# Performance work log

Hardware: AMD Instinct MI355X
Metric: run time of the kernel (lower is better)

## Reference

```python
import jax, jax.numpy as jnp
import numpy as np

N = 50000
E = 800000
F_IN = 128
HID = 16
HEADS = 8
CLS = 16
NEG_SLOPE = 0.2


def setup_inputs() -> dict:
    key = jax.random.key(0)
    ks = jax.random.split(key, 12)
    x = jax.random.normal(ks[0], (N, F_IN), dtype=jnp.float32)
    edge_index = jax.random.randint(ks[1], (2, E), 0, N, dtype=jnp.int32)
    s = 0.1
    W1 = jax.random.normal(ks[2], (F_IN, HEADS * HID), dtype=jnp.float32) * s
    att_src1 = jax.random.normal(ks[3], (HEADS, HID), dtype=jnp.float32) * s
    att_dst1 = jax.random.normal(ks[4], (HEADS, HID), dtype=jnp.float32) * s
    b1 = jax.random.normal(ks[5], (HEADS * HID,), dtype=jnp.float32) * s
    W2 = jax.random.normal(ks[6], (HEADS * HID, CLS), dtype=jnp.float32) * s
    att_src2 = jax.random.normal(ks[7], (1, CLS), dtype=jnp.float32) * s
    att_dst2 = jax.random.normal(ks[8], (1, CLS), dtype=jnp.float32) * s
    b2 = jax.random.normal(ks[9], (CLS,), dtype=jnp.float32) * s
    return {"x": x, "edge_index": edge_index, "W1": W1, "att_src1": att_src1,
            "att_dst1": att_dst1, "b1": b1, "W2": W2, "att_src2": att_src2,
            "att_dst2": att_dst2, "b2": b2}


def _gat_conv(x, src, dst, W, a_src, a_dst, b, heads, out_ch, concat):
    n = x.shape[0]
    h = (x @ W).reshape(n, heads, out_ch)                     # [N,H,C]
    alpha_src = (h * a_src[None]).sum(-1)                     # [N,H]
    alpha_dst = (h * a_dst[None]).sum(-1)                     # [N,H]
    e = jax.nn.leaky_relu(alpha_src[src] + alpha_dst[dst], NEG_SLOPE)  # [E,H]
    m = jax.lax.stop_gradient(jax.ops.segment_max(e, dst, num_segments=n))
    e = jnp.exp(e - m[dst])
    denom = jax.ops.segment_sum(e, dst, num_segments=n)
    alpha = e / (denom[dst] + 1e-16)                          # [E,H]
    msg = h[src] * alpha[:, :, None]                          # [E,H,C]
    out = jax.ops.segment_sum(msg, dst, num_segments=n)       # [N,H,C]
    out = out.reshape(n, heads * out_ch) if concat else out.mean(axis=1)
    return out + b


def reference(x, edge_index, W1, att_src1, att_dst1, b1, W2, att_src2, att_dst2, b2):
    # PyG GATConv default add_self_loops=True
    loop = jnp.arange(N, dtype=edge_index.dtype)
    src = jnp.concatenate([edge_index[0], loop])
    dst = jnp.concatenate([edge_index[1], loop])
    h = _gat_conv(x, src, dst, W1, att_src1, att_dst1, b1, HEADS, HID, True)
    h = jax.nn.elu(h)
    # dropout inactive (eval mode)
    out = _gat_conv(h, src, dst, W2, att_src2, att_dst2, b2, 1, CLS, False)
    return out
```

## Files before the change

### kernel.cpp

```cpp
#include <hip/hip_runtime.h>
#include <hip/hip_bf16.h>
#include <limits.h>
#include <math.h>

#define N 50000
#define E_ 800000
#define ETOT 850000
#define HH 128
#define HEADS 8
#define HID 16
#define CLS 16
#define NEG 0.2f
#define NB ((N + 255) / 256)

typedef unsigned short u16;
typedef unsigned int   u32;
typedef unsigned long long u64;
typedef short s8v __attribute__((ext_vector_type(8)));
typedef float f4v __attribute__((ext_vector_type(4)));

__device__ __forceinline__ u16 f2bu(float f){
  union{float f; u32 i;} c; c.f = f;
  u32 lsb = (c.i >> 16) & 1u;
  c.i += 0x7fffu + lsb;
  return (u16)(c.i >> 16);
}
__device__ __forceinline__ float bu2f(u16 u){
  union{u32 i; float f;} c; c.i = ((u32)u) << 16; return c.f;
}
__device__ __forceinline__ float blo(u32 u){ union{u32 i; float f;} c; c.i = u << 16; return c.f; }
__device__ __forceinline__ float bhi(u32 u){ union{u32 i; float f;} c; c.i = u & 0xffff0000u; return c.f; }

__global__ __launch_bounds__(256) void k_prepW(const float* __restrict__ W,
                                               u16* __restrict__ wth, u16* __restrict__ wtl){
  int i = blockIdx.x*256 + threadIdx.x;
  if(i >= 128*128) return;
  int k = i >> 7, c = i & 127;
  float v = W[i];
  u16 hi = f2bu(v);
  u16 lo = f2bu(v - bu2f(hi));
  wth[c*128 + k] = hi;
  wtl[c*128 + k] = lo;
}

__global__ __launch_bounds__(256) void k_link(const int* __restrict__ ei,
                                              int* __restrict__ head,
                                              int* __restrict__ srcv,
                                              int* __restrict__ nxt){
  int e = blockIdx.x*256 + threadIdx.x;
  if(e >= ETOT) return;
  int s, d;
  if(e < E_){ s = ei[e]; d = ei[E_ + e]; } else { s = d = e - E_; }
  int old = atomicExch(&head[d], e);
  srcv[e] = s;
  nxt[e]  = old;
}

#define GBM 64
__global__ __launch_bounds__(256) void k_gemm1m(const float* __restrict__ x,
                                                const u16* __restrict__ wth,
                                                const u16* __restrict__ wtl,
                                                u16* __restrict__ h1b){
  __shared__ u16 xh[GBM][40], xl[GBM][40];
  __shared__ u16 wh[128][40], wl[128][40];
  int tid  = threadIdx.x;
  int wv   = tid >> 6;
  int lane = tid & 63;
  int row0 = blockIdx.x * GBM;

  f4v acc[4][2];
  #pragma unroll
  for(int t=0;t<4;t++)
    #pragma unroll
    for(int u=0;u<2;u++) acc[t][u] = (f4v){0.f,0.f,0.f,0.f};

  int xr  = tid >> 2;
  int xkq = (tid & 3) * 8;
  int wc  = tid & 127;
  int wq  = (tid >> 7) * 8;
  int xrow = row0 + xr; if(xrow >= N) xrow = N-1;
  const float* xb = x + (size_t)xrow*128 + xkq;
  int fr = lane & 15, fg = lane >> 4;
  int kk = fg*8;

  for(int kc=0; kc<4; kc++){
    int k0 = kc*32;
    float4 v0 = *(const float4*)(xb + k0);
    float4 v1 = *(const float4*)(xb + k0 + 4);
    __syncthreads();
    {
      float vv[8] = {v0.x,v0.y,v0.z,v0.w,v1.x,v1.y,v1.z,v1.w};
      s8v H, L;
      #pragma unroll
      for(int j=0;j<8;j++){
        u16 h_ = f2bu(vv[j]);
        H[j] = (short)h_;
        L[j] = (short)f2bu(vv[j] - bu2f(h_));
      }
      *(s8v*)&xh[xr][xkq] = H;
      *(s8v*)&xl[xr][xkq] = L;
    }
    #pragma unroll
    for(int j=0;j<2;j++){
      int kq = wq + j*16;
      *(s8v*)&wh[wc][kq] = *(const s8v*)&wth[wc*128 + k0 + kq];
      *(s8v*)&wl[wc][kq] = *(const s8v*)&wtl[wc*128 + k0 + kq];
    }
    __syncthreads();
    s8v a_h[4], a_l[4], b_h[2], b_l[2];
    #pragma unroll
    for(int t=0;t<4;t++){
      a_h[t] = *(const s8v*)&xh[t*16 + fr][kk];
      a_l[t] = *(const s8v*)&xl[t*16 + fr][kk];
    }
    #pragma unroll
    for(int u=0;u<2;u++){
      int col = wv*32 + u*16 + fr;
      b_h[u] = *(const s8v*)&wh[col][kk];
      b_l[u] = *(const s8v*)&wl[col][kk];
    }
    #pragma unroll
    for(int t=0;t<4;t++){
      #pragma unroll
      for(int u=0;u<2;u++){
        acc[t][u] = __builtin_amdgcn_mfma_f32_16x16x32_bf16(a_h[t], b_h[u], acc[t][u], 0,0,0);
        acc[t][u] = __builtin_amdgcn_mfma_f32_16x16x32_bf16(a_h[t], b_l[u], acc[t][u], 0,0,0);
        acc[t][u] = __builtin_amdgcn_mfma_f32_16x16x32_bf16(a_l[t], b_h[u], acc[t][u], 0,0,0);
      }
    }
  }
  #pragma unroll
  for(int t=0;t<4;t++){
    #pragma unroll
    for(int j=0;j<4;j++){
      int row = row0 + t*16 + fg*4 + j;
      if(row < N){
        u16* dst = h1b + (size_t)row*128 + wv*32 + fr;
        dst[0]  = f2bu(acc[t][0][j]);
        dst[16] = f2bu(acc[t][1][j]);
      }
    }
  }
}

__global__ __launch_bounds__(256) void k_alpha1(const u16* __restrict__ h1b,
                                                const float* __restrict__ Asv,
                                                const float* __restrict__ Adv,
                                                float* __restrict__ as1,
                                                float* __restrict__ ad1){
  int id = blockIdx.x*256 + threadIdx.x;
  if(id >= N*HEADS) return;
  int i = id >> 3, h = id & 7;
  const uint4* hv = (const uint4*)(h1b + (size_t)i*HH + h*HID);
  uint4 u0 = hv[0], u1 = hv[1];
  float vals[16] = {blo(u0.x),bhi(u0.x),blo(u0.y),bhi(u0.y),
                    blo(u0.z),bhi(u0.z),blo(u0.w),bhi(u0.w),
                    blo(u1.x),bhi(u1.x),blo(u1.y),bhi(u1.y),
                    blo(u1.z),bhi(u1.z),blo(u1.w),bhi(u1.w)};
  float s=0.f, d=0.f;
  #pragma unroll
  for(int j=0;j<16;j++){
    s = fmaf(vals[j], Asv[h*HID+j], s);
    d = fmaf(vals[j], Adv[h*HID+j], d);
  }
  as1[id]=s; ad1[id]=d;
}

__global__ __launch_bounds__(256) void k_scan1walk(const int* __restrict__ head,
                                                   const int* __restrict__ nxt,
                                                   int* __restrict__ deg,
                                                   int* __restrict__ bsum){
  __shared__ int sm[256];
  int t = threadIdx.x;
  int i = blockIdx.x*256 + t;
  int cnt = 0;
  if(i < N){
    int e = head[i];
    while(e >= 0){ cnt++; e = nxt[e]; }
    deg[i] = cnt;
  }
  sm[t] = cnt;
  __syncthreads();
  #pragma unroll
  for(int ofs=128; ofs>0; ofs>>=1){
    if(t < ofs) sm[t] += sm[t+ofs];
    __syncthreads();
  }
  if(t == 0) bsum[blockIdx.x] = sm[0];
}

__global__ __launch_bounds__(256) void k_scan2(const int* __restrict__ bsum,
                                               int* __restrict__ boff,
                                               int* __restrict__ off){
  __shared__ int sm[256];
  int t = threadIdx.x;
  sm[t] = (t < NB) ? bsum[t] : 0;
  __syncthreads();
  #pragma unroll
  for(int ofs=1; ofs<256; ofs<<=1){
    int v = sm[t];
    int add = (t >= ofs) ? sm[t-ofs] : 0;
    __syncthreads();
    sm[t] = v + add;
    __syncthreads();
  }
  if(t < NB) boff[t] = (t == 0) ? 0 : sm[t-1];
  if(t == 255) off[N] = sm[NB-1];
}

__global__ __launch_bounds__(256) void k_scan3walk(const int* __restrict__ deg,
                                                   const int* __restrict__ boff,
                                                   const int* __restrict__ head,
                                                   const int* __restrict__ srcv,
                                                   const int* __restrict__ nxt,
                                                   int* __restrict__ off,
                                                   int* __restrict__ csr){
  __shared__ int sm[256];
  int t = threadIdx.x;
  int i = blockIdx.x*256 + t;
  int v0 = (i < N) ? deg[i] : 0;
  sm[t] = v0;
  __syncthreads();
  #pragma unroll
  for(int ofs=1; ofs<256; ofs<<=1){
    int v = sm[t];
    int add = (t >= ofs) ? sm[t-ofs] : 0;
    __syncthreads();
    sm[t] = v + add;
    __syncthreads();
  }
  if(i < N){
    int excl = boff[blockIdx.x] + sm[t] - v0;
    off[i] = excl;
    int e = head[i];
    int pos = excl;
    while(e >= 0){
      csr[pos++] = srcv[e];
      e = nxt[e];
    }
  }
}

#define CH 32
__global__ __launch_bounds__(256) void k_agg1(const int* __restrict__ off,
                                              const int* __restrict__ csr,
                                              const float* __restrict__ as1,
                                              const float* __restrict__ ad1,
                                              const u32* __restrict__ h1w,
                                              const float* __restrict__ b1,
                                              u32* __restrict__ helu_w){
  __shared__ float wsm[4][CH*8];
  __shared__ int   ssm[4][CH];
  int wv   = threadIdx.x >> 6;
  int lane = threadIdx.x & 63;
  int node = blockIdx.x*4 + wv;
  int beg = off[node], end = off[node+1];
  int h  = lane >> 3;
  int hh = lane & 7;
  int el = lane >> 3;
  float advA = ad1[node*8 + hh];
  float den = 0.f, num0 = 0.f, num1 = 0.f;
  float* wsw = wsm[wv];
  int*   ssw = ssm[wv];
  for(int base = beg; base < end; base += CH){
    int cnt = end - base; if(cnt > CH) cnt = CH;
    #pragma unroll
    for(int k=0;k<CH;k+=8){
      int e = el + k;
      if(e < cnt){
        int s = csr[base+e];
        if(hh == 0) ssw[e] = s;
        float v = as1[s*8+hh] + advA;
        v = v > 0.f ? v : NEG*v;
        wsw[e*8+hh] = __expf(v);
      }
    }
    int e = 0;
    for(; e+4 <= cnt; e += 4){
      int s0 = ssw[e], s1 = ssw[e+1], s2 = ssw[e+2], s3 = ssw[e+3];
      float w0 = wsw[e*8+h], w1 = wsw[e*8+8+h], w2 = wsw[e*8+16+h], w3 = wsw[e*8+24+h];
      u32 u0 = h1w[(size_t)s0*64 + lane];
      u32 u1 = h1w[(size_t)s1*64 + lane];
      u32 u2 = h1w[(size_t)s2*64 + lane];
      u32 u3 = h1w[(size_t)s3*64 + lane];
      den += (w0+w1)+(w2+w3);
      num0 = fmaf(w0, blo(u0), num0); num1 = fmaf(w0, bhi(u0), num1);
      num0 = fmaf(w1, blo(u1), num0); num1 = fmaf(w1, bhi(u1), num1);
      num0 = fmaf(w2, blo(u2), num0); num1 = fmaf(w2, bhi(u2), num1);
      num0 = fmaf(w3, blo(u3), num0); num1 = fmaf(w3, bhi(u3), num1);
    }
    for(; e < cnt; e++){
      int s = ssw[e];
      float w = wsw[e*8+h];
      u32 u = h1w[(size_t)s*64 + lane];
      den += w;
      num0 = fmaf(w, blo(u), num0);
      num1 = fmaf(w, bhi(u), num1);
    }
  }
  float2 bb = ((const float2*)b1)[lane];
  float inv = 1.f / (den + 1e-16f);
  float r0 = num0*inv + bb.x;
  float r1 = num1*inv + bb.y;
  r0 = r0 > 0.f ? r0 : expm1f(r0);
  r1 = r1 > 0.f ? r1 : expm1f(r1);
  helu_w[(size_t)node*64 + lane] = (u32)f2bu(r0) | ((u32)f2bu(r1) << 16);
}

__global__ __launch_bounds__(256) void k_gemm2(const u16* __restrict__ hb,
                                               const float* __restrict__ W2,
                                               const float* __restrict__ Asv,
                                               const float* __restrict__ Adv,
                                               u16* __restrict__ h2b,
                                               float* __restrict__ as2,
                                               float* __restrict__ ad2){
  __shared__ float Wl[128*16];
  int tid = threadIdx.x;
  const float4* W4 = (const float4*)W2;
  float4* Wl4 = (float4*)Wl;
  Wl4[tid]       = W4[tid];
  Wl4[tid + 256] = W4[tid + 256];
  __syncthreads();
  int i = blockIdx.x*16 + (tid >> 4);
  int c = tid & 15;
  if(i >= N) return;
  const uint4* h8 = (const uint4*)(hb + (size_t)i*HH);
  float acc = 0.f;
  #pragma unroll
  for(int ch=0; ch<16; ch++){
    uint4 u = h8[ch];
    int k = ch*8;
    acc = fmaf(blo(u.x), Wl[(k+0)*16+c], acc);
    acc = fmaf(bhi(u.x), Wl[(k+1)*16+c], acc);
    acc = fmaf(blo(u.y), Wl[(k+2)*16+c], acc);
    acc = fmaf(bhi(u.y), Wl[(k+3)*16+c], acc);
    acc = fmaf(blo(u.z), Wl[(k+4)*16+c], acc);
    acc = fmaf(bhi(u.z), Wl[(k+5)*16+c], acc);
    acc = fmaf(blo(u.w), Wl[(k+6)*16+c], acc);
    acc = fmaf(bhi(u.w), Wl[(k+7)*16+c], acc);
  }
  h2b[(size_t)i*CLS + c] = f2bu(acc);
  float ps = acc * Asv[c];
  float pd = acc * Adv[c];
  ps += __shfl_xor(ps,1); ps += __shfl_xor(ps,2); ps += __shfl_xor(ps,4); ps += __shfl_xor(ps,8);
  pd += __shfl_xor(pd,1); pd += __shfl_xor(pd,2); pd += __shfl_xor(pd,4); pd += __shfl_xor(pd,8);
  if(c == 0){ as2[i] = ps; ad2[i] = pd; }
}

__global__ __launch_bounds__(256) void k_agg2(const int* __restrict__ off,
                                              const int* __restrict__ csr,
                                              const float* __restrict__ as2,
                                              const float* __restrict__ ad2,
                                              const u32* __restrict__ h2w,
                                              const float* __restrict__ b2,
                                              float* __restrict__ outp){
  int t = threadIdx.x;
  int node = blockIdx.x*32 + (t >> 3);
  int c2 = t & 7;
  if(node >= N) return;
  int beg = off[node], end = off[node+1];
  float adv = ad2[node];
  float den = 0.f, num0 = 0.f, num1 = 0.f;
  for(int base = beg; base < end; base += 8){
    int cnt = end - base; if(cnt > 8) cnt = 8;
    float w_my = 0.f; int s_my = 0;
    if(c2 < cnt){
      s_my = csr[base + c2];
      float v = as2[s_my] + adv;
      v = v > 0.f ? v : NEG*v;
      w_my = __expf(v);
    }
    #pragma unroll
    for(int j=0; j<8; j++){
      if(j >= cnt) break;
      int src = (t & 56) | j;
      float w = __shfl(w_my, src);
      int   s = __shfl(s_my, src);
      u32 u = h2w[(size_t)s*8 + c2];
      den += w;
      num0 = fmaf(w, blo(u), num0);
      num1 = fmaf(w, bhi(u), num1);
    }
  }
  float inv = 1.f / (den + 1e-16f);
  float2 bb = ((const float2*)b2)[c2];
  float2 r;
  r.x = num0*inv + bb.x;
  r.y = num1*inv + bb.y;
  ((float2*)outp)[(size_t)node*8 + c2] = r;
}

extern "C" void kernel_launch(void* const* d_in, const int* in_sizes, int n_in,
                              void* d_out, int out_size, void* d_ws, size_t ws_size,
                              hipStream_t stream){
  const float* x     = (const float*)d_in[0];
  const int*   ei    = (const int*)  d_in[1];
  const float* W1    = (const float*)d_in[2];
  const float* av_s1 = (const float*)d_in[3];
  const float* av_d1 = (const float*)d_in[4];
  const float* b1    = (const float*)d_in[5];
  const float* W2    = (const float*)d_in[6];
  const float* av_s2 = (const float*)d_in[7];
  const float* av_d2 = (const float*)d_in[8];
  const float* b2    = (const float*)d_in[9];
  float* outp = (float*)d_out;

  char* p = (char*)d_ws;
  auto alloc = [&](size_t bytes){ char* q = p; p += (bytes + 255) & ~(size_t)255; return q; };
  u16*   h1b    = (u16*)  alloc((size_t)N*HH*2);
  u16*   helu_b = (u16*)  alloc((size_t)N*HH*2);
  u16*   h2b    = (u16*)  alloc((size_t)N*CLS*2);
  float* as1    = (float*)alloc((size_t)N*HEADS*4);
  float* ad1    = (float*)alloc((size_t)N*HEADS*4);
  float* as2    = (float*)alloc((size_t)N*4);
  float* ad2    = (float*)alloc((size_t)N*4);
  int*   deg    = (int*)  alloc((size_t)N*4);
  int*   head   = (int*)  alloc((size_t)N*4);
  int*   off    = (int*)  alloc((size_t)(N+1)*4);
  int*   csr    = (int*)  alloc((size_t)ETOT*4);
  int*   srcv   = (int*)  alloc((size_t)ETOT*4);
  int*   nxt    = (int*)  alloc((size_t)ETOT*4);
  u16*   wth    = (u16*)  alloc((size_t)128*128*2);
  u16*   wtl    = (u16*)  alloc((size_t)128*128*2);
  int*   bsum   = (int*)  alloc((size_t)NB*4);
  int*   boff   = (int*)  alloc((size_t)NB*4);

  hipMemsetAsync(head, 0xFF, (size_t)N*4, stream);

  k_link<<<(ETOT+255)/256, 256, 0, stream>>>(ei, head, srcv, nxt);
  k_prepW<<<(128*128+255)/256, 256, 0, stream>>>(W1, wth, wtl);

  k_gemm1m<<<(N+GBM-1)/GBM, 256, 0, stream>>>(x, wth, wtl, h1b);
  k_alpha1<<<(N*HEADS+255)/256, 256, 0, stream>>>(h1b, av_s1, av_d1, as1, ad1);

  k_scan1walk<<<NB, 256, 0, stream>>>(head, nxt, deg, bsum);
  k_scan2<<<1, 256, 0, stream>>>(bsum, boff, off);
  k_scan3walk<<<NB, 256, 0, stream>>>(deg, boff, head, srcv, nxt, off, csr);

  k_agg1<<<N/4, 256, 0, stream>>>(off, csr, as1, ad1, (const u32*)h1b, b1, (u32*)helu_b);

  k_gemm2<<<(N+15)/16, 256, 0, stream>>>(helu_b, W2, av_s2, av_d2, h2b, as2, ad2);
  k_agg2<<<(N+31)/32, 256, 0, stream>>>(off, csr, as2, ad2, (const u32*)h2b, b2, outp);
}
```

Measured before the change: 171.1 us.

## Merge independent kernels via block-index dispatch and fold scan2 into scan3

Runs the edge linking in extra blocks of the first GEMM launch, and the degree walk in extra blocks of the alpha kernel, so independent work shares one launch. The single-block middle scan is dropped: each scan3 block now reduces the preceding block sums itself. k_agg1 also uses a larger edge chunk (64) and issues 8 gathers per unrolled step. This is meant to cut launch overhead and serial gaps between small kernels and to raise memory-level parallelism in the aggregation. The cost is bigger fused kernels with more register and shared memory use, and atomics running at the same time as the GEMM.

```diff
diff --git a/kernel.cpp b/kernel.cpp
--- a/kernel.cpp
+++ b/kernel.cpp
@@ -12,10 +12,13 @@
 #define CLS 16
 #define NEG 0.2f
 #define NB ((N + 255) / 256)
+#define GBM 64
+#define GEMM_NB ((N + GBM - 1) / GBM)
+#define LINK_NB ((ETOT + 255) / 256)
+#define A1_NB ((N*HEADS + 255) / 256)
 
 typedef unsigned short u16;
 typedef unsigned int   u32;
-typedef unsigned long long u64;
 typedef short s8v __attribute__((ext_vector_type(8)));
 typedef float f4v __attribute__((ext_vector_type(4)));
 
@@ -43,26 +46,27 @@
   wtl[c*128 + k] = lo;
 }
 
-__global__ __launch_bounds__(256) void k_link(const int* __restrict__ ei,
-                                              int* __restrict__ head,
-                                              int* __restrict__ srcv,
-                                              int* __restrict__ nxt){
-  int e = blockIdx.x*256 + threadIdx.x;
-  if(e >= ETOT) return;
-  int s, d;
-  if(e < E_){ s = ei[e]; d = ei[E_ + e]; } else { s = d = e - E_; }
-  int old = atomicExch(&head[d], e);
-  srcv[e] = s;
-  nxt[e]  = old;
-}
-
-#define GBM 64
-__global__ __launch_bounds__(256) void k_gemm1m(const float* __restrict__ x,
-                                                const u16* __restrict__ wth,
-                                                const u16* __restrict__ wtl,
-                                                u16* __restrict__ h1b){
+__global__ __launch_bounds__(256) void k_gemm1link(const float* __restrict__ x,
+                                                   const u16* __restrict__ wth,
+                                                   const u16* __restrict__ wtl,
+                                                   u16* __restrict__ h1b,
+                                                   const int* __restrict__ ei,
+                                                   int* __restrict__ head,
+                                                   int* __restrict__ srcv,
+                                                   int* __restrict__ nxt){
   __shared__ u16 xh[GBM][40], xl[GBM][40];
   __shared__ u16 wh[128][40], wl[128][40];
+  if(blockIdx.x >= GEMM_NB){
+    int e = (blockIdx.x - GEMM_NB)*256 + threadIdx.x;
+    if(e < ETOT){
+      int s, d;
+      if(e < E_){ s = ei[e]; d = ei[E_ + e]; } else { s = d = e - E_; }
+      int old = atomicExch(&head[d], e);
+      srcv[e] = s;
+      nxt[e]  = old;
+    }
+    return;
+  }
   int tid  = threadIdx.x;
   int wv   = tid >> 6;
   int lane = tid & 63;
@@ -143,12 +147,36 @@
   }
 }
 
-__global__ __launch_bounds__(256) void k_alpha1(const u16* __restrict__ h1b,
-                                                const float* __restrict__ Asv,
-                                                const float* __restrict__ Adv,
-                                                float* __restrict__ as1,
-                                                float* __restrict__ ad1){
-  int id = blockIdx.x*256 + threadIdx.x;
+__global__ __launch_bounds__(256) void k_alphascan1(const u16* __restrict__ h1b,
+                                                    const float* __restrict__ Asv,
+                                                    const float* __restrict__ Adv,
+                                                    float* __restrict__ as1,
+                                                    float* __restrict__ ad1,
+                                                    const int* __restrict__ head,
+                                                    const int* __restrict__ nxt,
+                                                    int* __restrict__ deg,
+                                                    int* __restrict__ bsum){
+  __shared__ int sm[256];
+  if(blockIdx.x < NB){
+    int t = threadIdx.x;
+    int i = blockIdx.x*256 + t;
+    int cnt = 0;
+    if(i < N){
+      int e = head[i];
+      while(e >= 0){ cnt++; e = nxt[e]; }
+      deg[i] = cnt;
+    }
+    sm[t] = cnt;
+    __syncthreads();
+    #pragma unroll
+    for(int ofs=128; ofs>0; ofs>>=1){
+      if(t < ofs) sm[t] += sm[t+ofs];
+      __syncthreads();
+    }
+    if(t == 0) bsum[blockIdx.x] = sm[0];
+    return;
+  }
+  int id = (blockIdx.x - NB)*256 + threadIdx.x;
   if(id >= N*HEADS) return;
   int i = id >> 3, h = id & 7;
   const uint4* hv = (const uint4*)(h1b + (size_t)i*HH + h*HID);
@@ -166,57 +194,24 @@
   as1[id]=s; ad1[id]=d;
 }
 
-__global__ __launch_bounds__(256) void k_scan1walk(const int* __restrict__ head,
-                                                   const int* __restrict__ nxt,
-                                                   int* __restrict__ deg,
-                                                   int* __restrict__ bsum){
-  __shared__ int sm[256];
-  int t = threadIdx.x;
-  int i = blockIdx.x*256 + t;
-  int cnt = 0;
-  if(i < N){
-    int e = head[i];
-    while(e >= 0){ cnt++; e = nxt[e]; }
-    deg[i] = cnt;
-  }
-  sm[t] = cnt;
-  __syncthreads();
-  #pragma unroll
-  for(int ofs=128; ofs>0; ofs>>=1){
-    if(t < ofs) sm[t] += sm[t+ofs];
-    __syncthreads();
-  }
-  if(t == 0) bsum[blockIdx.x] = sm[0];
-}
-
-__global__ __launch_bounds__(256) void k_scan2(const int* __restrict__ bsum,
-                                               int* __restrict__ boff,
-                                               int* __restrict__ off){
-  __shared__ int sm[256];
-  int t = threadIdx.x;
-  sm[t] = (t < NB) ? bsum[t] : 0;
-  __syncthreads();
-  #pragma unroll
-  for(int ofs=1; ofs<256; ofs<<=1){
-    int v = sm[t];
-    int add = (t >= ofs) ? sm[t-ofs] : 0;
-    __syncthreads();
-    sm[t] = v + add;
-    __syncthreads();
-  }
-  if(t < NB) boff[t] = (t == 0) ? 0 : sm[t-1];
-  if(t == 255) off[N] = sm[NB-1];
-}
-
 __global__ __launch_bounds__(256) void k_scan3walk(const int* __restrict__ deg,
-                                                   const int* __restrict__ boff,
+                                                   const int* __restrict__ bsum,
                                                    const int* __restrict__ head,
                                                    const int* __restrict__ srcv,
                                                    const int* __restrict__ nxt,
                                                    int* __restrict__ off,
                                                    int* __restrict__ csr){
+  __shared__ int red[256];
   __shared__ int sm[256];
   int t = threadIdx.x;
+  red[t] = (t < blockIdx.x) ? bsum[t] : 0;
+  __syncthreads();
+  #pragma unroll
+  for(int ofs=128; ofs>0; ofs>>=1){
+    if(t < ofs) red[t] += red[t+ofs];
+    __syncthreads();
+  }
+  int boff = red[0];
   int i = blockIdx.x*256 + t;
   int v0 = (i < N) ? deg[i] : 0;
   sm[t] = v0;
@@ -230,8 +225,9 @@
     __syncthreads();
   }
   if(i < N){
-    int excl = boff[blockIdx.x] + sm[t] - v0;
+    int excl = boff + sm[t] - v0;
     off[i] = excl;
+    if(i == N-1) off[N] = excl + v0;
     int e = head[i];
     int pos = excl;
     while(e >= 0){
@@ -241,7 +237,7 @@
   }
 }
 
-#define CH 32
+#define CH 64
 __global__ __launch_bounds__(256) void k_agg1(const int* __restrict__ off,
                                               const int* __restrict__ csr,
                                               const float* __restrict__ as1,
@@ -262,6 +258,7 @@
   float den = 0.f, num0 = 0.f, num1 = 0.f;
   float* wsw = wsm[wv];
   int*   ssw = ssm[wv];
+  const u32* hp = h1w + lane;
   for(int base = beg; base < end; base += CH){
     int cnt = end - base; if(cnt > CH) cnt = CH;
     #pragma unroll
@@ -276,23 +273,23 @@
       }
     }
     int e = 0;
-    for(; e+4 <= cnt; e += 4){
-      int s0 = ssw[e], s1 = ssw[e+1], s2 = ssw[e+2], s3 = ssw[e+3];
-      float w0 = wsw[e*8+h], w1 = wsw[e*8+8+h], w2 = wsw[e*8+16+h], w3 = wsw[e*8+24+h];
-      u32 u0 = h1w[(size_t)s0*64 + lane];
-      u32 u1 = h1w[(size_t)s1*64 + lane];
-      u32 u2 = h1w[(size_t)s2*64 + lane];
-      u32 u3 = h1w[(size_t)s3*64 + lane];
-      den += (w0+w1)+(w2+w3);
-      num0 = fmaf(w0, blo(u0), num0); num1 = fmaf(w0, bhi(u0), num1);
-      num0 = fmaf(w1, blo(u1), num0); num1 = fmaf(w1, bhi(u1), num1);
-      num0 = fmaf(w2, blo(u2), num0); num1 = fmaf(w2, bhi(u2), num1);
-      num0 = fmaf(w3, blo(u3), num0); num1 = fmaf(w3, bhi(u3), num1);
+    for(; e+8 <= cnt; e += 8){
+      int ss[8]; float ww[8]; u32 uu[8];
+      #pragma unroll
+      for(int j=0;j<8;j++){ ss[j] = ssw[e+j]; ww[j] = wsw[(e+j)*8+h]; }
+      #pragma unroll
+      for(int j=0;j<8;j++){ uu[j] = hp[(size_t)ss[j]*64]; }
+      #pragma unroll
+      for(int j=0;j<8;j++){
+        den += ww[j];
+        num0 = fmaf(ww[j], blo(uu[j]), num0);
+        num1 = fmaf(ww[j], bhi(uu[j]), num1);
+      }
     }
     for(; e < cnt; e++){
       int s = ssw[e];
       float w = wsw[e*8+h];
-      u32 u = h1w[(size_t)s*64 + lane];
+      u32 u = hp[(size_t)s*64];
       den += w;
       num0 = fmaf(w, blo(u), num0);
       num1 = fmaf(w, bhi(u), num1);
@@ -423,19 +420,16 @@
   u16*   wth    = (u16*)  alloc((size_t)128*128*2);
   u16*   wtl    = (u16*)  alloc((size_t)128*128*2);
   int*   bsum   = (int*)  alloc((size_t)NB*4);
-  int*   boff   = (int*)  alloc((size_t)NB*4);
 
   hipMemsetAsync(head, 0xFF, (size_t)N*4, stream);
 
-  k_link<<<(ETOT+255)/256, 256, 0, stream>>>(ei, head, srcv, nxt);
   k_prepW<<<(128*128+255)/256, 256, 0, stream>>>(W1, wth, wtl);
 
-  k_gemm1m<<<(N+GBM-1)/GBM, 256, 0, stream>>>(x, wth, wtl, h1b);
-  k_alpha1<<<(N*HEADS+255)/256, 256, 0, stream>>>(h1b, av_s1, av_d1, as1, ad1);
-
-  k_scan1walk<<<NB, 256, 0, stream>>>(head, nxt, deg, bsum);
-  k_scan2<<<1, 256, 0, stream>>>(bsum, boff, off);
-  k_scan3walk<<<NB, 256, 0, stream>>>(deg, boff, head, srcv, nxt, off, csr);
+  k_gemm1link<<<GEMM_NB + LINK_NB, 256, 0, stream>>>(x, wth, wtl, h1b, ei, head, srcv, nxt);
+
+  k_alphascan1<<<NB + A1_NB, 256, 0, stream>>>(h1b, av_s1, av_d1, as1, ad1, head, nxt, deg, bsum);
+
+  k_scan3walk<<<NB, 256, 0, stream>>>(deg, bsum, head, srcv, nxt, off, csr);
 
   k_agg1<<<N/4, 256, 0, stream>>>(off, csr, as1, ad1, (const u32*)h1b, b1, (u32*)helu_b);
 
```

Result: faster. 160.4 us (-6.2%).
